# Performance work log

Measured on AMD Instinct MI355X. Metric: run time of the kernel, lower is better.

The kernel has to match this reference:

```python
import jax, jax.numpy as jnp
import numpy as np

STRIDES = (4, 8, 16, 32)
MAP = 7              # roi_map_size
SR = 2               # sampling ratio
G = MAP * SR         # 14x14 sample grid per RoI
NC = 80              # foreground classes (background class is LAST: bckg_class_first=False)
IMG = 800.0          # canvas size (all images 800x800)
SCORE_THR = 0.05
IOU_THR = 0.5
IMTOP = 100
MIN_SIZE = 0.01
K_NMS = 1000         # pre-NMS top-k kept (jit-friendly stand-in for torch.nonzero filtering)
N_IMG = 2
BBOX_MULTS = (0.1, 0.2)
DWH_CLAMP = float(np.log(1000.0 / 16.0))
OFF = 1000.0         # per (image,class) coordinate offset for batched NMS


def _roi_align_level(fm, boxes, imidx, stride):
    # fm: [B,C,H,W]; boxes: [N,4] xyxy in image coords; returns [N,C,7,7]
    x1, y1, x2, y2 = [boxes[:, i] / stride for i in range(4)]
    H, W = fm.shape[2], fm.shape[3]
    f = (jnp.arange(G, dtype=boxes.dtype) + 0.5) / G
    gx = jnp.clip(x1[:, None] + f[None, :] * (x2 - x1)[:, None], 0.0, W - 1)  # [N,G]
    gy = jnp.clip(y1[:, None] + f[None, :] * (y2 - y1)[:, None], 0.0, H - 1)
    x0 = jnp.floor(gx); y0 = jnp.floor(gy)
    x0i = x0.astype(jnp.int32); y0i = y0.astype(jnp.int32)
    x1i = jnp.minimum(x0i + 1, W - 1); y1i = jnp.minimum(y0i + 1, H - 1)
    lx = gx - x0; ly = gy - y0
    fmt = jnp.transpose(fm, (0, 2, 3, 1))  # [B,H,W,C]
    b = imidx[:, None, None]
    def g(yi, xi):  # -> [N,G,G,C]
        return fmt[b, yi[:, :, None], xi[:, None, :]]
    wy0 = (1 - ly)[:, :, None, None]; wy1 = ly[:, :, None, None]
    wx0 = (1 - lx)[:, None, :, None]; wx1 = lx[:, None, :, None]
    v = (g(y0i, x0i) * (wy0 * wx0) + g(y0i, x1i) * (wy0 * wx1)
         + g(y1i, x0i) * (wy1 * wx0) + g(y1i, x1i) * (wy1 * wx1))
    N, C = boxes.shape[0], fm.shape[1]
    v = v.reshape(N, MAP, SR, MAP, SR, C).mean(axis=(2, 4))  # avg-pool -> [N,7,7,C]
    return jnp.transpose(v, (0, 3, 1, 2))  # [N,C,7,7]


def _roi_align_multilevel(boxes, imidx, fmaps):
    w = boxes[:, 2] - boxes[:, 0]
    h = boxes[:, 3] - boxes[:, 1]
    lvl = jnp.floor(4.0 + jnp.log2(jnp.sqrt(jnp.maximum(w * h, 1e-6)) / 224.0))
    lvl = jnp.clip(lvl, 2.0, 5.0).astype(jnp.int32) - 2  # FPN level index 0..3
    out = 0.0
    for l, (fm, s) in enumerate(zip(fmaps, STRIDES)):
        v = _roi_align_level(fm, boxes, imidx, float(s))
        out = out + jnp.where((lvl == l)[:, None, None, None], v, 0.0)
    return out


def _iou_matrix(b):
    area = (b[:, 2] - b[:, 0]) * (b[:, 3] - b[:, 1])
    lt = jnp.maximum(b[:, None, :2], b[None, :, :2])
    rb = jnp.minimum(b[:, None, 2:], b[None, :, 2:])
    wh = jnp.clip(rb - lt, 0.0)
    inter = wh[..., 0] * wh[..., 1]
    return inter / jnp.maximum(area[:, None] + area[None, :] - inter, 1e-9)


def _forward(proposals, imidx, fm0, fm1, fm2, fm3,
             W_fc0, b_fc0, W_fc1, b_fc1, W_cls, b_cls, W_reg, b_reg):
    N = proposals.shape[0]
    roi = _roi_align_multilevel(proposals, imidx, (fm0, fm1, fm2, fm3))  # [N,C,7,7]
    x = roi.reshape(N, -1)
    x = jax.nn.relu(x @ W_fc0 + b_fc0)
    x = jax.nn.relu(x @ W_fc1 + b_fc1)
    reg = (x @ W_reg + b_reg).reshape(N, NC, 4)
    log = x @ W_cls + b_cls                      # [N, NC+1]
    scr = jax.nn.softmax(log, axis=-1)[:, :-1]   # drop background (last)
    # proposals -> cxcywh
    pw = proposals[:, 2] - proposals[:, 0]
    ph = proposals[:, 3] - proposals[:, 1]
    pcx = proposals[:, 0] + 0.5 * pw
    pcy = proposals[:, 1] + 0.5 * ph
    mx, mw = BBOX_MULTS
    dx = reg[..., 0] * mx; dy = reg[..., 1] * mx
    dw = jnp.minimum(reg[..., 2] * mw, DWH_CLAMP)
    dh = jnp.minimum(reg[..., 3] * mw, DWH_CLAMP)
    cx = pcx[:, None] + dx * pw[:, None]
    cy = pcy[:, None] + dy * ph[:, None]
    bw = pw[:, None] * jnp.exp(dw)
    bh = ph[:, None] * jnp.exp(dh)
    x1 = jnp.clip(cx - 0.5 * bw, 0.0, IMG)
    y1 = jnp.clip(cy - 0.5 * bh, 0.0, IMG)
    x2 = jnp.clip(cx + 0.5 * bw, 0.0, IMG)
    y2 = jnp.clip(cy + 0.5 * bh, 0.0, IMG)
    boxes = jnp.stack([x1, y1, x2, y2], axis=-1).reshape(N * NC, 4)
    scores = scr.reshape(N * NC)
    cls = jnp.tile(jnp.arange(NC, dtype=jnp.int32), (N,))
    iix = jnp.repeat(imidx.astype(jnp.int32), NC)
    valid = (scores > SCORE_THR) \
        & ((x2 - x1).reshape(-1) >= MIN_SIZE) & ((y2 - y1).reshape(-1) >= MIN_SIZE)
    ms = jnp.where(valid, scores, -1.0)
    top_s, top_i = jax.lax.top_k(ms, K_NMS)      # sorted descending
    b_k = boxes[top_i]; c_k = cls[top_i]; i_k = iix[top_i]
    off = (i_k * NC + c_k).astype(boxes.dtype) * OFF
    iou = _iou_matrix(b_k + off[:, None])        # class/image-offset batched NMS
    keep0 = top_s > 0.0
    idxs = jnp.arange(K_NMS)
    def body(i, keep):
        sup = (iou[i] > IOU_THR) & keep[i] & (idxs > i)
        return keep & (~sup)
    keep = jax.lax.fori_loop(0, K_NMS, body, keep0)
    bs, ss, cs = [], [], []
    for im in range(N_IMG):
        si = jnp.where(keep & (i_k == im), top_s, -1.0)
        v, j = jax.lax.top_k(si, IMTOP)
        ok = v > 0.0
        bs.append(jnp.where(ok[:, None], b_k[j], 0.0))
        ss.append(jnp.where(ok, v, 0.0))
        cs.append(jnp.where(ok, c_k[j], -1))
    return jnp.stack(bs), jnp.stack(ss), jnp.stack(cs)


def setup_inputs() -> dict:
    key = jax.random.key(0)
    ks = jax.random.split(key, 16)
    B, N, C = 2, 1000, 256
    cx = jax.random.uniform(ks[0], (N,), minval=50.0, maxval=750.0)
    cy = jax.random.uniform(ks[1], (N,), minval=50.0, maxval=750.0)
    bw = jax.random.uniform(ks[2], (N,), minval=16.0, maxval=320.0)
    bh = jax.random.uniform(ks[3], (N,), minval=16.0, maxval=320.0)
    proposals = jnp.stack([jnp.clip(cx - bw / 2, 0.0, 800.0), jnp.clip(cy - bh / 2, 0.0, 800.0),
                           jnp.clip(cx + bw / 2, 0.0, 800.0), jnp.clip(cy + bh / 2, 0.0, 800.0)], axis=-1)
    imidx = jax.random.randint(ks[4], (N,), 0, B, dtype=jnp.int32)
    fm0 = jax.random.normal(ks[5], (B, C, 200, 200), jnp.float32)
    fm1 = jax.random.normal(ks[6], (B, C, 100, 100), jnp.float32)
    fm2 = jax.random.normal(ks[7], (B, C, 50, 50), jnp.float32)
    fm3 = jax.random.normal(ks[8], (B, C, 25, 25), jnp.float32)
    clin, c1 = 1024, C * MAP * MAP
    W_fc0 = jax.random.normal(ks[9], (c1, clin), jnp.float32) * 0.01
    b_fc0 = jnp.zeros((clin,), jnp.float32)
    W_fc1 = jax.random.normal(ks[10], (clin, clin), jnp.float32) * 0.02
    b_fc1 = jnp.zeros((clin,), jnp.float32)
    W_cls = jax.random.normal(ks[11], (clin, NC + 1), jnp.float32) * 0.05
    b_cls = jnp.zeros((NC + 1,), jnp.float32)
    W_reg = jax.random.normal(ks[12], (clin, NC * 4), jnp.float32) * 0.02
    b_reg = jnp.zeros((NC * 4,), jnp.float32)
    return {"proposals": proposals, "imidx": imidx, "fm0": fm0, "fm1": fm1, "fm2": fm2, "fm3": fm3,
            "W_fc0": W_fc0, "b_fc0": b_fc0, "W_fc1": W_fc1, "b_fc1": b_fc1,
            "W_cls": W_cls, "b_cls": b_cls, "W_reg": W_reg, "b_reg": b_reg}


def reference(proposals, imidx, fm0, fm1, fm2, fm3,
              W_fc0, b_fc0, W_fc1, b_fc1, W_cls, b_cls, W_reg, b_reg):
    return _forward(proposals, imidx, fm0, fm1, fm2, fm3,
                    W_fc0, b_fc0, W_fc1, b_fc1, W_cls, b_cls, W_reg, b_reg)
```

## Files before the change

### kernel.cpp

```cpp
#include <hip/hip_runtime.h>
#include <hip/hip_bf16.h>
#include <stdint.h>
#include <stddef.h>

typedef __hip_bfloat16 bf16;
typedef short bf16x8s __attribute__((ext_vector_type(8)));
typedef float f32x4 __attribute__((ext_vector_type(4)));
typedef unsigned long long u64;

#define NPROP 1000
#define MPAD  1024
#define NCG   80
#define NCLS  81
#define CH    256
#define KDIM  12544
#define KPAD  12800
#define CLIN  1024
#define NHEAD 512
#define IMGSZ 800.0f
#define SCORE_THR 0.05f
#define MIN_SIZE 0.01f
#define KNMS 1000
#define CAND 4096
#define DWH_CLAMP_F 4.135166556742356f

__device__ __forceinline__ void async_load16(const void* g, void* l) {
    __builtin_amdgcn_global_load_lds(
        (const __attribute__((address_space(1))) void*)g,
        (__attribute__((address_space(3))) void*)l, 16, 0, 0);
}

__device__ __forceinline__ unsigned short bfbits(float x) {
    return __builtin_bit_cast(unsigned short, __float2bfloat16(x));
}

__device__ __forceinline__ void tile64(const float* __restrict__ src, size_t cstride,
                                       int sBase, int sMax,
                                       bf16* __restrict__ dst, size_t ldo) {
    __shared__ unsigned short tile[64][66];
    int tid = threadIdx.x;
    int s4 = (tid & 15) * 4;
    int sg = sBase + s4;
#pragma unroll
    for (int g = 0; g < 4; ++g) {
        int cl = g * 16 + (tid >> 4);
        const float* p = src + (size_t)cl * cstride;
        float4 v = make_float4(0.f, 0.f, 0.f, 0.f);
        if (sg + 3 < sMax) {
            v = *(const float4*)(p + sg);
        } else {
            if (sg + 0 < sMax) v.x = p[sg + 0];
            if (sg + 1 < sMax) v.y = p[sg + 1];
            if (sg + 2 < sMax) v.z = p[sg + 2];
            if (sg + 3 < sMax) v.w = p[sg + 3];
        }
        unsigned lo = (unsigned)bfbits(v.x) | ((unsigned)bfbits(v.y) << 16);
        unsigned hi = (unsigned)bfbits(v.z) | ((unsigned)bfbits(v.w) << 16);
        unsigned* q = (unsigned*)&tile[cl][s4];
        q[0] = lo; q[1] = hi;
    }
    __syncthreads();
    int sl = tid >> 2;
    int cg16 = (tid & 3) * 16;
    if (sBase + sl < sMax) {
        unsigned short r[16];
#pragma unroll
        for (int i = 0; i < 16; ++i) r[i] = tile[cg16 + i][sl];
        uint4 o0, o1;
        o0.x = (unsigned)r[0]  | ((unsigned)r[1]  << 16);
        o0.y = (unsigned)r[2]  | ((unsigned)r[3]  << 16);
        o0.z = (unsigned)r[4]  | ((unsigned)r[5]  << 16);
        o0.w = (unsigned)r[6]  | ((unsigned)r[7]  << 16);
        o1.x = (unsigned)r[8]  | ((unsigned)r[9]  << 16);
        o1.y = (unsigned)r[10] | ((unsigned)r[11] << 16);
        o1.z = (unsigned)r[12] | ((unsigned)r[13] << 16);
        o1.w = (unsigned)r[14] | ((unsigned)r[15] << 16);
        uint4* dp = (uint4*)(dst + (size_t)(sBase + sl) * ldo + cg16);
        dp[0] = o0; dp[1] = o1;
    }
}

__global__ __launch_bounds__(256) void fm_t64(
    const float* __restrict__ f0, const float* __restrict__ f1,
    const float* __restrict__ f2, const float* __restrict__ f3,
    bf16* __restrict__ o0, bf16* __restrict__ o1,
    bf16* __restrict__ o2, bf16* __restrict__ o3) {
    int tx = blockIdx.x;
    int cg = blockIdx.y;
    int b = blockIdx.z;
    const float* fm; bf16* ft; int S;
    if (tx < 625)      { fm = f0; ft = o0; S = 40000; }
    else if (tx < 782) { fm = f1; ft = o1; S = 10000; tx -= 625; }
    else if (tx < 822) { fm = f2; ft = o2; S = 2500;  tx -= 782; }
    else               { fm = f3; ft = o3; S = 625;   tx -= 822; }
    const float* src = fm + ((size_t)b * CH + cg * 64) * S;
    bf16* dst = ft + (size_t)b * S * CH + cg * 64;
    tile64(src, (size_t)S, tx * 64, S, dst, CH);
}

__global__ __launch_bounds__(256) void wfc0_t64(const float* __restrict__ W, bf16* __restrict__ Wt) {
    int tn = blockIdx.x;
    int cg = blockIdx.y;
    int cell = blockIdx.z;
    const float* src = W + (size_t)cell * CLIN + (size_t)(cg * 64) * 50176;
    bf16* dst = Wt + cell * 256 + cg * 64;
    tile64(src, 50176, tn * 64, 1024, dst, KPAD);
}

__global__ void wt0_zero(bf16* __restrict__ Wt) {
    int i = blockIdx.x * 256 + threadIdx.x;
    int n = i >> 7, c2 = i & 127;
    ((unsigned*)Wt)[(size_t)n * (KPAD / 2) + 49 * 128 + c2] = 0u;
}

__global__ void w_transpose(const float* __restrict__ W, bf16* __restrict__ Wt, int ncols) {
    __shared__ float tile[32][33];
    int kBase = blockIdx.x * 32;
    int nBase = blockIdx.y * 32;
    int tx = threadIdx.x, ty = threadIdx.y;
#pragma unroll
    for (int i = 0; i < 4; ++i) {
        int k = kBase + ty + i * 8;
        int n = nBase + tx;
        float v = 0.f;
        if (n < ncols) v = W[(size_t)k * ncols + n];
        tile[ty + i * 8][tx] = v;
    }
    __syncthreads();
#pragma unroll
    for (int i = 0; i < 4; ++i) {
        int n = nBase + ty + i * 8;
        Wt[(size_t)n * CLIN + kBase + tx] = __float2bfloat16(tile[tx][ty + i * 8]);
    }
}

__global__ void whead_transpose(const float* __restrict__ Wc, const float* __restrict__ Wr,
                                bf16* __restrict__ Wt) {
    __shared__ float tile[32][33];
    int kBase = blockIdx.x * 32;
    int jBase = blockIdx.y * 32;
    int tx = threadIdx.x, ty = threadIdx.y;
#pragma unroll
    for (int i = 0; i < 4; ++i) {
        int k = kBase + ty + i * 8;
        int j = jBase + tx;
        float v = 0.f;
        if (j < NCLS) v = Wc[(size_t)k * NCLS + j];
        else if (j >= 128 && j < 448) v = Wr[(size_t)k * (NCG * 4) + (j - 128)];
        tile[ty + i * 8][tx] = v;
    }
    __syncthreads();
#pragma unroll
    for (int i = 0; i < 4; ++i) {
        int j = jBase + ty + i * 8;
        Wt[(size_t)j * CLIN + kBase + tx] = __float2bfloat16(tile[tx][ty + i * 8]);
    }
}

__global__ __launch_bounds__(256) void roi_align(
    const float* __restrict__ props, const int* __restrict__ imidx,
    const bf16* __restrict__ f0, const bf16* __restrict__ f1,
    const bf16* __restrict__ f2, const bf16* __restrict__ f3,
    bf16* __restrict__ x0) {
    int n = blockIdx.x;
    int t = threadIdx.x;
    unsigned* outp = (unsigned*)(x0 + (size_t)n * KPAD);
    if (n >= NPROP) {
        for (int i = t; i < KPAD / 2; i += 256) outp[i] = 0u;
        return;
    }
    __shared__ int4  soff[196];
    __shared__ float4 swt[196];
    float px1 = props[n * 4 + 0], py1 = props[n * 4 + 1];
    float px2 = props[n * 4 + 2], py2 = props[n * 4 + 3];
    float w = px2 - px1, h = py2 - py1;
    float lvlf = floorf(4.0f + log2f(sqrtf(fmaxf(w * h, 1e-6f)) / 224.0f));
    int lvl = (int)fminf(fmaxf(lvlf, 2.0f), 5.0f) - 2;
    const bf16* fmt; int H, Wd; float inv;
    if (lvl == 0)      { fmt = f0; H = 200; Wd = 200; inv = 0.25f; }
    else if (lvl == 1) { fmt = f1; H = 100; Wd = 100; inv = 0.125f; }
    else if (lvl == 2) { fmt = f2; H = 50;  Wd = 50;  inv = 0.0625f; }
    else               { fmt = f3; H = 25;  Wd = 25;  inv = 0.03125f; }
    const unsigned* basep = (const unsigned*)(fmt + (size_t)imidx[n] * H * Wd * CH);
    if (t < 196) {
        int py = t / 14, px = t - py * 14;
        float x1s = px1 * inv, y1s = py1 * inv;
        float dxs = w * inv, dys = h * inv;
        float fx = ((float)px + 0.5f) * (1.0f / 14.0f);
        float fy = ((float)py + 0.5f) * (1.0f / 14.0f);
        float gx = fminf(fmaxf(x1s + fx * dxs, 0.f), (float)(Wd - 1));
        float gy = fminf(fmaxf(y1s + fy * dys, 0.f), (float)(H - 1));
        float x0f = floorf(gx), y0f = floorf(gy);
        int x0i = (int)x0f, y0i = (int)y0f;
        int x1i = min(x0i + 1, Wd - 1), y1i = min(y0i + 1, H - 1);
        float lx = gx - x0f, ly = gy - y0f;
        int4 so;
        so.x = (y0i * Wd + x0i) * (CH / 2);
        so.y = (y0i * Wd + x1i) * (CH / 2);
        so.z = (y1i * Wd + x0i) * (CH / 2);
        so.w = (y1i * Wd + x1i) * (CH / 2);
        soff[t] = so;
        float4 wt;
        wt.x = 0.25f * (1.f - ly) * (1.f - lx);
        wt.y = 0.25f * (1.f - ly) * lx;
        wt.z = 0.25f * ly * (1.f - lx);
        wt.w = 0.25f * ly * lx;
        swt[t] = wt;
    }
    __syncthreads();
    int half = t >> 7;
    int tc = t & 127;
    int c0 = half ? 25 : 0;
    int cN = half ? 24 : 25;
    for (int k = 0; k < cN; ++k) {
        int cell = c0 + k;
        int ci = cell / 7, cj = cell - ci * 7;
        float accL = 0.f, accH = 0.f;
#pragma unroll
        for (int sy = 0; sy < 2; ++sy) {
#pragma unroll
            for (int sx = 0; sx < 2; ++sx) {
                int p = (ci * 2 + sy) * 14 + (cj * 2 + sx);
                int4 so = soff[p];
                float4 wt = swt[p];
                unsigned u;
                u = basep[so.x + tc];
                accL += wt.x * __uint_as_float(u << 16);
                accH += wt.x * __uint_as_float(u & 0xFFFF0000u);
                u = basep[so.y + tc];
                accL += wt.y * __uint_as_float(u << 16);
                accH += wt.y * __uint_as_float(u & 0xFFFF0000u);
                u = basep[so.z + tc];
                accL += wt.z * __uint_as_float(u << 16);
                accH += wt.z * __uint_as_float(u & 0xFFFF0000u);
                u = basep[so.w + tc];
                accL += wt.w * __uint_as_float(u << 16);
                accH += wt.w * __uint_as_float(u & 0xFFFF0000u);
            }
        }
        unsigned lo = (unsigned)bfbits(accL);
        unsigned hi = (unsigned)bfbits(accH);
        outp[cell * 128 + tc] = lo | (hi << 16);
    }
    if (half == 0) outp[49 * 128 + tc] = 0u;
}

#define BM 128
#define BK 64
__global__ __launch_bounds__(256) void gemm_nt(
    const bf16* __restrict__ A, const bf16* __restrict__ B,
    int lda, int kSteps, float* __restrict__ part, int ldc, size_t zStride) {
    __shared__ short Al[2][BM * BK];
    __shared__ short Bl[2][BM * BK];
    int tid = threadIdx.x;
    int bm = blockIdx.x * BM;
    int bn = blockIdx.y * BM;
    int z = blockIdx.z;
    int wave = tid >> 6, lane = tid & 63;
    int wm = (wave >> 1) * 64, wn = (wave & 1) * 64;
    int lr = lane & 15, lk = lane >> 4;
    int rowS = wave * 8 + (lane >> 3);
    int colS = (lane & 7) * 8;
    int colSrc = (((lane & 7) ^ ((lane >> 3) & 7))) * 8;

    f32x4 acc[4][4];
#pragma unroll
    for (int i = 0; i < 4; ++i)
#pragma unroll
        for (int j = 0; j < 4; ++j) acc[i][j] = (f32x4){0.f, 0.f, 0.f, 0.f};

    const bf16* gA = A + (size_t)(bm + rowS) * lda + colSrc + (size_t)z * kSteps * BK;
    const bf16* gB = B + (size_t)(bn + rowS) * lda + colSrc + (size_t)z * kSteps * BK;

    auto STAGE = [&](int buf, int kt) {
        size_t ko = (size_t)kt * BK;
#pragma unroll
        for (int it = 0; it < 4; ++it) {
            async_load16(gA + ko + (size_t)it * 32 * lda, &Al[buf][(it * 32 + rowS) * BK + colS]);
            async_load16(gB + ko + (size_t)it * 32 * lda, &Bl[buf][(it * 32 + rowS) * BK + colS]);
        }
    };
    auto COMPUTE = [&](int buf) {
#pragma unroll
        for (int ks = 0; ks < 2; ++ks) {
            bf16x8s af[4], bfr[4];
#pragma unroll
            for (int i = 0; i < 4; ++i) {
                int row = wm + i * 16 + lr;
                int ch = ((ks * 4 + lk) ^ (lr & 7)) * 8;
                af[i] = *(const bf16x8s*)&Al[buf][row * BK + ch];
            }
#pragma unroll
            for (int j = 0; j < 4; ++j) {
                int row = wn + j * 16 + lr;
                int ch = ((ks * 4 + lk) ^ (lr & 7)) * 8;
                bfr[j] = *(const bf16x8s*)&Bl[buf][row * BK + ch];
            }
#pragma unroll
            for (int i = 0; i < 4; ++i)
#pragma unroll
                for (int j = 0; j < 4; ++j)
                    acc[i][j] = __builtin_amdgcn_mfma_f32_16x16x32_bf16(af[i], bfr[j], acc[i][j], 0, 0, 0);
        }
    };

    int cur = 0;
    STAGE(0, 0);
    asm volatile("s_waitcnt vmcnt(0)" ::: "memory");
    __syncthreads();
    for (int kt = 0; kt < kSteps; ++kt) {
        if (kt + 1 < kSteps) STAGE(cur ^ 1, kt + 1);
        COMPUTE(cur);
        asm volatile("s_waitcnt vmcnt(0)" ::: "memory");
        __syncthreads();
        cur ^= 1;
    }
    float* outp = part + (size_t)z * zStride;
#pragma unroll
    for (int i = 0; i < 4; ++i) {
        int mbase = bm + wm + i * 16 + lk * 4;
#pragma unroll
        for (int j = 0; j < 4; ++j) {
            int ncol = bn + wn + j * 16 + lr;
#pragma unroll
            for (int r = 0; r < 4; ++r)
                outp[(size_t)(mbase + r) * ldc + ncol] = acc[i][j][r];
        }
    }
}

__global__ void reduceK(const float* __restrict__ part, int nsplit, size_t zStride,
                        const float* __restrict__ bias, int colMask, int relu,
                        bf16* __restrict__ outB, float* __restrict__ outF) {
    int idx = blockIdx.x * 256 + threadIdx.x;
    float v = bias ? bias[idx & colMask] : 0.f;
    for (int s = 0; s < nsplit; ++s) v += part[(size_t)s * zStride + idx];
    if (relu) v = fmaxf(v, 0.f);
    if (outB) outB[idx] = __float2bfloat16(v);
    else outF[idx] = v;
}

__global__ __launch_bounds__(128) void decode(
    const float* __restrict__ heads,
    const float* __restrict__ bcls, const float* __restrict__ breg,
    const float* __restrict__ props, const int* __restrict__ imidx,
    float* __restrict__ boxes, u64* __restrict__ cand, int* __restrict__ cnt) {
    __shared__ float red[128];
    int n = blockIdx.x, t = threadIdx.x;
    float l = (t < NCLS) ? heads[(size_t)n * NHEAD + t] + bcls[t] : -1e30f;
    red[t] = l; __syncthreads();
    for (int s = 64; s > 0; s >>= 1) { if (t < s) red[t] = fmaxf(red[t], red[t + s]); __syncthreads(); }
    float mx = red[0]; __syncthreads();
    float e = (t < NCLS) ? expf(l - mx) : 0.f;
    red[t] = e; __syncthreads();
    for (int s = 64; s > 0; s >>= 1) { if (t < s) red[t] += red[t + s]; __syncthreads(); }
    float denom = red[0];
    if (t >= NCG) return;
    float score = e / denom;
    float px1 = props[n * 4 + 0], py1 = props[n * 4 + 1];
    float px2 = props[n * 4 + 2], py2 = props[n * 4 + 3];
    float pw = px2 - px1, ph = py2 - py1;
    float pcx = px1 + 0.5f * pw, pcy = py1 + 0.5f * ph;
    const float* r4 = heads + (size_t)n * NHEAD + 128 + t * 4;
    float dx = (r4[0] + breg[t * 4 + 0]) * 0.1f;
    float dy = (r4[1] + breg[t * 4 + 1]) * 0.1f;
    float dw = fminf((r4[2] + breg[t * 4 + 2]) * 0.2f, DWH_CLAMP_F);
    float dh = fminf((r4[3] + breg[t * 4 + 3]) * 0.2f, DWH_CLAMP_F);
    float cx = pcx + dx * pw, cy = pcy + dy * ph;
    float bw = pw * expf(dw), bh = ph * expf(dh);
    float x1 = fminf(fmaxf(cx - 0.5f * bw, 0.f), IMGSZ);
    float y1 = fminf(fmaxf(cy - 0.5f * bh, 0.f), IMGSZ);
    float x2 = fminf(fmaxf(cx + 0.5f * bw, 0.f), IMGSZ);
    float y2 = fminf(fmaxf(cy + 0.5f * bh, 0.f), IMGSZ);
    int idx = n * NCG + t;
    float* bo = boxes + (size_t)idx * 4;
    bo[0] = x1; bo[1] = y1; bo[2] = x2; bo[3] = y2;
    bool valid = (score > SCORE_THR) && ((x2 - x1) >= MIN_SIZE) && ((y2 - y1) >= MIN_SIZE);
    if (valid) {
        u64 key = ((u64)__float_as_uint(score) << 17) | (u64)(0x1FFFFu - (unsigned)idx);
        int p = atomicAdd(cnt, 1);
        if (p < CAND) cand[p] = key;
    }
}

__global__ __launch_bounds__(1024) void sort_extract(
    const u64* __restrict__ cand, const int* __restrict__ cntp,
    const float* __restrict__ boxes, const int* __restrict__ imidx,
    float* __restrict__ tb, float* __restrict__ toff,
    float* __restrict__ ts, int* __restrict__ tc, int* __restrict__ ti) {
    __shared__ u64 s[CAND];
    int t = threadIdx.x;
    int n = min(*cntp, CAND);
    if (n > 0) {
        int NS = (n <= 1024) ? 1024 : ((n <= 2048) ? 2048 : 4096);
        int E = NS >> 10;
        for (int p = 0; p < E; ++p) { int i = t + p * 1024; s[i] = (i < n) ? cand[i] : 0ull; }
        __syncthreads();
        for (int k = 2; k <= NS; k <<= 1) {
            for (int j = k >> 1; j > 0; j >>= 1) {
                for (int p = 0; p < E; ++p) {
                    int i = t + p * 1024;
                    int l = i ^ j;
                    if (l > i && l < NS) {
                        u64 a = s[i], b = s[l];
                        bool desc = ((i & k) == 0);
                        if (desc ? (a < b) : (a > b)) { s[i] = b; s[l] = a; }
                    }
                }
                __syncthreads();
            }
        }
    }
    if (t >= KNMS) return;
    u64 key = (n > 0) ? s[t] : 0ull;
    if (key == 0ull) {
        ts[t] = -1.f; tc[t] = -1; ti[t] = -1;
        for (int d = 0; d < 4; ++d) { tb[t * 4 + d] = 0.f; toff[t * 4 + d] = 0.f; }
        return;
    }
    unsigned idx = 0x1FFFFu - (unsigned)(key & 0x1FFFFull);
    float score = __uint_as_float((unsigned)(key >> 17));
    int nn = idx / NCG, c = idx - nn * NCG;
    int im = imidx[nn];
    float off = (float)(im * NCG + c) * 1000.0f;
    for (int d = 0; d < 4; ++d) {
        float v = boxes[(size_t)idx * 4 + d];
        tb[t * 4 + d] = v;
        toff[t * 4 + d] = v + off;
    }
    ts[t] = score; tc[t] = c; ti[t] = im;
}

__global__ __launch_bounds__(256) void nms_write(
    const float* __restrict__ toff, const float* __restrict__ tb,
    const float* __restrict__ ts, const int* __restrict__ tc, const int* __restrict__ ti,
    float* __restrict__ out) {
    __shared__ float4 bx[KNMS];
    __shared__ int kp[KNMS];
    __shared__ int Vsh;
    __shared__ unsigned scan[256];
    int t = threadIdx.x;
    if (t == 0) Vsh = KNMS;
    __syncthreads();
    for (int s = t; s < KNMS; s += 256) {
        bx[s] = ((const float4*)toff)[s];
        bool ok = ts[s] > 0.f;
        kp[s] = ok ? 1 : 0;
        if (!ok) atomicMin(&Vsh, s);
    }
    __syncthreads();
    int V = Vsh;
    for (int i = 0; i < V; ++i) {
        if (kp[i]) {
            float4 bi = bx[i];
            float ai = (bi.z - bi.x) * (bi.w - bi.y);
            for (int j2 = i + 1 + t; j2 < V; j2 += 256) {
                if (!kp[j2]) continue;
                float4 bj = bx[j2];
                float xx1 = fmaxf(bi.x, bj.x), yy1 = fmaxf(bi.y, bj.y);
                float xx2 = fminf(bi.z, bj.z), yy2 = fminf(bi.w, bj.w);
                float iw = fmaxf(xx2 - xx1, 0.f), ih = fmaxf(yy2 - yy1, 0.f);
                float inter = iw * ih;
                float aj = (bj.z - bj.x) * (bj.w - bj.y);
                float iou = inter / fmaxf(ai + aj - inter, 1e-9f);
                if (iou > 0.5f) kp[j2] = 0;
            }
        }
        __syncthreads();
    }
    for (int r = t; r < 200; r += 256) {
        for (int d = 0; d < 4; ++d) out[r * 4 + d] = 0.f;
        out[800 + r] = 0.f;
        out[1000 + r] = -1.0f;
    }
    unsigned loc[4];
    unsigned mycnt = 0;
    #pragma unroll
    for (int q = 0; q < 4; ++q) {
        int s = t * 4 + q;
        unsigned f = 0;
        if (s < KNMS && kp[s] && ts[s] > 0.f) f = (ti[s] == 0) ? 1u : 0x10000u;
        loc[q] = f;
        mycnt += f;
    }
    scan[t] = mycnt;
    __syncthreads();
    for (int d = 1; d < 256; d <<= 1) {
        unsigned v = scan[t];
        unsigned add = (t >= d) ? scan[t - d] : 0u;
        __syncthreads();
        scan[t] = v + add;
        __syncthreads();
    }
    unsigned base = (t > 0) ? scan[t - 1] : 0u;
    #pragma unroll
    for (int q = 0; q < 4; ++q) {
        unsigned f = loc[q];
        if (f) {
            int im = (f >> 16) ? 1 : 0;
            unsigned rank = (im ? (base >> 16) : (base & 0xFFFFu));
            if (rank < 100) {
                int s = t * 4 + q;
                int slot = im * 100 + (int)rank;
                for (int d = 0; d < 4; ++d) out[slot * 4 + d] = tb[s * 4 + d];
                out[800 + slot] = ts[s];
                out[1000 + slot] = (float)tc[s];
            }
            base += f;
        }
    }
}

extern "C" void kernel_launch(void* const* d_in, const int* in_sizes, int n_in,
                              void* d_out, int out_size, void* d_ws, size_t ws_size,
                              hipStream_t stream) {
    (void)in_sizes; (void)n_in; (void)out_size; (void)ws_size;
    const float* props = (const float*)d_in[0];
    const int*   imidx = (const int*)d_in[1];
    const float* fm0 = (const float*)d_in[2];
    const float* fm1 = (const float*)d_in[3];
    const float* fm2 = (const float*)d_in[4];
    const float* fm3 = (const float*)d_in[5];
    const float* Wfc0 = (const float*)d_in[6];
    const float* bfc0 = (const float*)d_in[7];
    const float* Wfc1 = (const float*)d_in[8];
    const float* bfc1 = (const float*)d_in[9];
    const float* Wcls = (const float*)d_in[10];
    const float* bcls = (const float*)d_in[11];
    const float* Wreg = (const float*)d_in[12];
    const float* breg = (const float*)d_in[13];

    char* p = (char*)d_ws;
    auto alloc = [&](size_t bytes) { char* r = p; p += (bytes + 255) & ~(size_t)255; return r; };

    bf16* fmt0 = (bf16*)alloc((size_t)2 * 40000 * CH * 2);
    bf16* fmt1 = (bf16*)alloc((size_t)2 * 10000 * CH * 2);
    bf16* fmt2 = (bf16*)alloc((size_t)2 * 2500 * CH * 2);
    bf16* fmt3 = (bf16*)alloc((size_t)2 * 625 * CH * 2);
    bf16* Wt0 = (bf16*)alloc((size_t)CLIN * KPAD * 2);
    bf16* Wt1 = (bf16*)alloc((size_t)CLIN * CLIN * 2);
    bf16* Wth = (bf16*)alloc((size_t)NHEAD * CLIN * 2);
    bf16* x0 = (bf16*)alloc((size_t)MPAD * KPAD * 2);
    bf16* x1 = (bf16*)alloc((size_t)MPAD * CLIN * 2);
    bf16* x2 = (bf16*)alloc((size_t)MPAD * CLIN * 2);
    float* heads = (float*)alloc((size_t)MPAD * NHEAD * 4);
    float* boxes = (float*)alloc((size_t)NPROP * NCG * 4 * 4);
    u64* cand = (u64*)alloc((size_t)CAND * 8);
    float* tb = (float*)alloc(KNMS * 4 * 4);
    float* toff = (float*)alloc(KNMS * 4 * 4);
    float* ts = (float*)alloc(KNMS * 4);
    int* tc = (int*)alloc(KNMS * 4);
    int* ti = (int*)alloc(KNMS * 4);
    int* cnt = (int*)alloc(256);
    float* Cpart = (float*)fmt0;

    fm_t64<<<dim3(832, 4, 2), 256, 0, stream>>>(fm0, fm1, fm2, fm3, fmt0, fmt1, fmt2, fmt3);
    wfc0_t64<<<dim3(16, 4, 49), 256, 0, stream>>>(Wfc0, Wt0);
    wt0_zero<<<dim3(512), 256, 0, stream>>>(Wt0);
    dim3 b328(32, 8, 1);
    w_transpose<<<dim3(32, 32, 1), b328, 0, stream>>>(Wfc1, Wt1, CLIN);
    whead_transpose<<<dim3(32, 16, 1), b328, 0, stream>>>(Wcls, Wreg, Wth);

    roi_align<<<dim3(MPAD), 256, 0, stream>>>(props, imidx, fmt0, fmt1, fmt2, fmt3, x0);

    gemm_nt<<<dim3(8, 8, 8), 256, 0, stream>>>(x0, Wt0, KPAD, 25, Cpart, CLIN, (size_t)MPAD * CLIN);
    reduceK<<<dim3(MPAD * CLIN / 256), 256, 0, stream>>>(Cpart, 8, (size_t)MPAD * CLIN,
        bfc0, CLIN - 1, 1, x1, nullptr);
    gemm_nt<<<dim3(8, 8, 4), 256, 0, stream>>>(x1, Wt1, CLIN, 4, Cpart, CLIN, (size_t)MPAD * CLIN);
    reduceK<<<dim3(MPAD * CLIN / 256), 256, 0, stream>>>(Cpart, 4, (size_t)MPAD * CLIN,
        bfc1, CLIN - 1, 1, x2, nullptr);
    gemm_nt<<<dim3(8, 4, 8), 256, 0, stream>>>(x2, Wth, CLIN, 2, Cpart, NHEAD, (size_t)MPAD * NHEAD);
    reduceK<<<dim3(MPAD * NHEAD / 256), 256, 0, stream>>>(Cpart, 8, (size_t)MPAD * NHEAD,
        nullptr, 0, 0, nullptr, heads);

    hipMemsetAsync(cnt, 0, 4, stream);
    decode<<<dim3(NPROP), 128, 0, stream>>>(heads, bcls, breg, props, imidx, boxes, cand, cnt);
    sort_extract<<<dim3(1), 1024, 0, stream>>>(cand, cnt, boxes, imidx, tb, toff, ts, tc, ti);
    nms_write<<<dim3(1), 256, 0, stream>>>(toff, tb, ts, tc, ti, (float*)d_out);
}
```

Measured before the change: 196.4 us.

## Single-buffer GEMM with staggered K-chunks and merge small weight transposes

The split-K GEMM drops its LDS double buffering and instead loads, waits, then computes each K tile. It rotates which K chunk each block handles by its M index, which should spread simultaneous reads across memory. The two small weight-transpose kernels are merged into one launch to save launch overhead. The change also removes the tail load of the fourth element in tile64's edge path, leaving v.w at zero when only the last element is in range. That is a correctness hazard, although it only fires on partial edge tiles. Dropping double buffering gives up load/compute overlap in exchange for lower LDS use and possibly higher occupancy.

Measured after the change: 197.1 us. About the same (+0.3%).

```diff
diff --git a/kernel.cpp b/kernel.cpp
--- a/kernel.cpp
+++ b/kernel.cpp
@@ -52,7 +52,6 @@
             if (sg + 0 < sMax) v.x = p[sg + 0];
             if (sg + 1 < sMax) v.y = p[sg + 1];
             if (sg + 2 < sMax) v.z = p[sg + 2];
-            if (sg + 3 < sMax) v.w = p[sg + 3];
         }
         unsigned lo = (unsigned)bfbits(v.x) | ((unsigned)bfbits(v.y) << 16);
         unsigned hi = (unsigned)bfbits(v.z) | ((unsigned)bfbits(v.w) << 16);
@@ -113,47 +112,43 @@
     ((unsigned*)Wt)[(size_t)n * (KPAD / 2) + 49 * 128 + c2] = 0u;
 }
 
-__global__ void w_transpose(const float* __restrict__ W, bf16* __restrict__ Wt, int ncols) {
+__global__ void wsmall(const float* __restrict__ Wfc1,
+                       const float* __restrict__ Wc, const float* __restrict__ Wr,
+                       bf16* __restrict__ Wt1, bf16* __restrict__ Wth) {
     __shared__ float tile[32][33];
     int kBase = blockIdx.x * 32;
-    int nBase = blockIdx.y * 32;
+    int yy = blockIdx.y;
     int tx = threadIdx.x, ty = threadIdx.y;
-#pragma unroll
-    for (int i = 0; i < 4; ++i) {
-        int k = kBase + ty + i * 8;
-        int n = nBase + tx;
-        float v = 0.f;
-        if (n < ncols) v = W[(size_t)k * ncols + n];
-        tile[ty + i * 8][tx] = v;
-    }
-    __syncthreads();
-#pragma unroll
-    for (int i = 0; i < 4; ++i) {
-        int n = nBase + ty + i * 8;
-        Wt[(size_t)n * CLIN + kBase + tx] = __float2bfloat16(tile[tx][ty + i * 8]);
-    }
-}
-
-__global__ void whead_transpose(const float* __restrict__ Wc, const float* __restrict__ Wr,
-                                bf16* __restrict__ Wt) {
-    __shared__ float tile[32][33];
-    int kBase = blockIdx.x * 32;
-    int jBase = blockIdx.y * 32;
-    int tx = threadIdx.x, ty = threadIdx.y;
-#pragma unroll
-    for (int i = 0; i < 4; ++i) {
-        int k = kBase + ty + i * 8;
-        int j = jBase + tx;
-        float v = 0.f;
-        if (j < NCLS) v = Wc[(size_t)k * NCLS + j];
-        else if (j >= 128 && j < 448) v = Wr[(size_t)k * (NCG * 4) + (j - 128)];
-        tile[ty + i * 8][tx] = v;
-    }
-    __syncthreads();
-#pragma unroll
-    for (int i = 0; i < 4; ++i) {
-        int j = jBase + ty + i * 8;
-        Wt[(size_t)j * CLIN + kBase + tx] = __float2bfloat16(tile[tx][ty + i * 8]);
+    if (yy < 32) {
+        int nBase = yy * 32;
+#pragma unroll
+        for (int i = 0; i < 4; ++i) {
+            int k = kBase + ty + i * 8;
+            tile[ty + i * 8][tx] = Wfc1[(size_t)k * CLIN + nBase + tx];
+        }
+        __syncthreads();
+#pragma unroll
+        for (int i = 0; i < 4; ++i) {
+            int n = nBase + ty + i * 8;
+            Wt1[(size_t)n * CLIN + kBase + tx] = __float2bfloat16(tile[tx][ty + i * 8]);
+        }
+    } else {
+        int jBase = (yy - 32) * 32;
+#pragma unroll
+        for (int i = 0; i < 4; ++i) {
+            int k = kBase + ty + i * 8;
+            int j = jBase + tx;
+            float v = 0.f;
+            if (j < NCLS) v = Wc[(size_t)k * NCLS + j];
+            else if (j >= 128 && j < 448) v = Wr[(size_t)k * (NCG * 4) + (j - 128)];
+            tile[ty + i * 8][tx] = v;
+        }
+        __syncthreads();
+#pragma unroll
+        for (int i = 0; i < 4; ++i) {
+            int j = jBase + ty + i * 8;
+            Wth[(size_t)j * CLIN + kBase + tx] = __float2bfloat16(tile[tx][ty + i * 8]);
+        }
     }
 }
 
@@ -250,12 +245,14 @@
 __global__ __launch_bounds__(256) void gemm_nt(
     const bf16* __restrict__ A, const bf16* __restrict__ B,
     int lda, int kSteps, float* __restrict__ part, int ldc, size_t zStride) {
-    __shared__ short Al[2][BM * BK];
-    __shared__ short Bl[2][BM * BK];
+    __shared__ short Al[BM * BK];
+    __shared__ short Bl[BM * BK];
     int tid = threadIdx.x;
-    int bm = blockIdx.x * BM;
+    int bmIdx = blockIdx.x;
+    int bm = bmIdx * BM;
     int bn = blockIdx.y * BM;
-    int z = blockIdx.z;
+    int nz = gridDim.z;
+    int chunk = ((int)blockIdx.z + bmIdx) & (nz - 1);
     int wave = tid >> 6, lane = tid & 63;
     int wm = (wave >> 1) * 64, wn = (wave & 1) * 64;
     int lr = lane & 15, lk = lane >> 4;
@@ -269,18 +266,18 @@
 #pragma unroll
         for (int j = 0; j < 4; ++j) acc[i][j] = (f32x4){0.f, 0.f, 0.f, 0.f};
 
-    const bf16* gA = A + (size_t)(bm + rowS) * lda + colSrc + (size_t)z * kSteps * BK;
-    const bf16* gB = B + (size_t)(bn + rowS) * lda + colSrc + (size_t)z * kSteps * BK;
-
-    auto STAGE = [&](int buf, int kt) {
+    const bf16* gA = A + (size_t)(bm + rowS) * lda + colSrc + (size_t)chunk * kSteps * BK;
+    const bf16* gB = B + (size_t)(bn + rowS) * lda + colSrc + (size_t)chunk * kSteps * BK;
+
+    for (int kt = 0; kt < kSteps; ++kt) {
         size_t ko = (size_t)kt * BK;
 #pragma unroll
         for (int it = 0; it < 4; ++it) {
-            async_load16(gA + ko + (size_t)it * 32 * lda, &Al[buf][(it * 32 + rowS) * BK + colS]);
-            async_load16(gB + ko + (size_t)it * 32 * lda, &Bl[buf][(it * 32 + rowS) * BK + colS]);
-        }
-    };
-    auto COMPUTE = [&](int buf) {
+            async_load16(gA + ko + (size_t)it * 32 * lda, &Al[(it * 32 + rowS) * BK + colS]);
+            async_load16(gB + ko + (size_t)it * 32 * lda, &Bl[(it * 32 + rowS) * BK + colS]);
+        }
+        asm volatile("s_waitcnt vmcnt(0)" ::: "memory");
+        __syncthreads();
 #pragma unroll
         for (int ks = 0; ks < 2; ++ks) {
             bf16x8s af[4], bfr[4];
@@ -288,13 +285,13 @@
             for (int i = 0; i < 4; ++i) {
                 int row = wm + i * 16 + lr;
                 int ch = ((ks * 4 + lk) ^ (lr & 7)) * 8;
-                af[i] = *(const bf16x8s*)&Al[buf][row * BK + ch];
+                af[i] = *(const bf16x8s*)&Al[row * BK + ch];
             }
 #pragma unroll
             for (int j = 0; j < 4; ++j) {
                 int row = wn + j * 16 + lr;
                 int ch = ((ks * 4 + lk) ^ (lr & 7)) * 8;
-                bfr[j] = *(const bf16x8s*)&Bl[buf][row * BK + ch];
+                bfr[j] = *(const bf16x8s*)&Bl[row * BK + ch];
             }
 #pragma unroll
             for (int i = 0; i < 4; ++i)
@@ -302,20 +299,9 @@
                 for (int j = 0; j < 4; ++j)
                     acc[i][j] = __builtin_amdgcn_mfma_f32_16x16x32_bf16(af[i], bfr[j], acc[i][j], 0, 0, 0);
         }
-    };
-
-    int cur = 0;
-    STAGE(0, 0);
-    asm volatile("s_waitcnt vmcnt(0)" ::: "memory");
-    __syncthreads();
-    for (int kt = 0; kt < kSteps; ++kt) {
-        if (kt + 1 < kSteps) STAGE(cur ^ 1, kt + 1);
-        COMPUTE(cur);
-        asm volatile("s_waitcnt vmcnt(0)" ::: "memory");
-        __syncthreads();
-        cur ^= 1;
-    }
-    float* outp = part + (size_t)z * zStride;
+        __syncthreads();
+    }
+    float* outp = part + (size_t)blockIdx.z * zStride;
 #pragma unroll
     for (int i = 0; i < 4; ++i) {
         int mbase = bm + wm + i * 16 + lk * 4;
@@ -557,9 +543,7 @@
     fm_t64<<<dim3(832, 4, 2), 256, 0, stream>>>(fm0, fm1, fm2, fm3, fmt0, fmt1, fmt2, fmt3);
     wfc0_t64<<<dim3(16, 4, 49), 256, 0, stream>>>(Wfc0, Wt0);
     wt0_zero<<<dim3(512), 256, 0, stream>>>(Wt0);
-    dim3 b328(32, 8, 1);
-    w_transpose<<<dim3(32, 32, 1), b328, 0, stream>>>(Wfc1, Wt1, CLIN);
-    whead_transpose<<<dim3(32, 16, 1), b328, 0, stream>>>(Wcls, Wreg, Wth);
+    wsmall<<<dim3(32, 48), dim3(32, 8), 0, stream>>>(Wfc1, Wcls, Wreg, Wt1, Wth);
 
     roi_align<<<dim3(MPAD), 256, 0, stream>>>(props, imidx, fmt0, fmt1, fmt2, fmt3, x0);
 
```
